# Kernel tuning notes

Measured on AMD Instinct MI355X. Metric: run time of the kernel, lower is better.

## Reference

```python
import jax, jax.numpy as jnp
import numpy as np

NPOINT, RADIUS, SIGMA, K = 1024, 0.1, 0.05, 32
KDE_K = 128  # N_points default of kernel_density_estimation_ball


def setup_inputs() -> dict:
    key = jax.random.key(0)
    ks = jax.random.split(key, 9)
    B, N, C = 4, 4096, 16

    def glorot(k, shape):
        fan_in, fan_out = shape
        return jax.random.normal(k, shape, jnp.float32) * jnp.sqrt(2.0 / (fan_in + fan_out))

    return {
        'xyz': jax.random.uniform(ks[0], (B, N, 3), jnp.float32),      # unit cube
        'feature': jax.random.normal(ks[1], (B, N, C), jnp.float32),
        'w_mlp0': glorot(ks[2], (3 + C, 128)),
        'w_mlp1': glorot(ks[3], (128, 128)),
        'w_mlp2': glorot(ks[4], (128, 256)),
        'w_wn': glorot(ks[5], (3, 32)),
        'w_nl0': glorot(ks[6], (1, 16)),
        'w_nl1': glorot(ks[7], (16, 1)),
        'w_np': glorot(ks[8], (32, 256)),
    }


def _pdist2(a, b):
    # squared pairwise distances [B, M, N]
    return (jnp.sum(a * a, -1)[:, :, None] + jnp.sum(b * b, -1)[:, None, :]
            - 2.0 * jnp.einsum('bmd,bnd->bmn', a, b))


def _fps(xyz, npoint):
    # farthest point sampling, seeded at index 0 (matches CUDA op semantics)
    B, N, _ = xyz.shape

    def step(carry, _):
        min_d, last = carry
        p = jnp.take_along_axis(xyz, last[:, None, None], axis=1)  # [B,1,3]
        d = jnp.sum((xyz - p) ** 2, -1)                            # [B,N]
        min_d = jnp.minimum(min_d, d)
        nxt = jnp.argmax(min_d, axis=1).astype(jnp.int32)
        return (min_d, nxt), nxt

    init = (jnp.full((B, N), jnp.inf, xyz.dtype), jnp.zeros((B,), jnp.int32))
    _, rest = jax.lax.scan(step, init, None, length=npoint - 1)
    return jnp.concatenate([jnp.zeros((B, 1), jnp.int32), rest.T], axis=1)  # [B,npoint]


def _ball_query(xyz, radius, k):
    # first-k-in-index-order neighbors with d2 < r^2, padded with first hit
    B, N, _ = xyz.shape
    d2 = _pdist2(xyz, xyz)
    in_ball = d2 < radius * radius                 # self always included
    j = jnp.arange(N, dtype=jnp.int32)
    keys = jnp.where(in_ball, j, j + N)            # in-ball indices sort first
    _, idx = jax.lax.top_k(-keys, k)               # k smallest keys -> positions j
    cnt = jnp.minimum(jnp.sum(in_ball, axis=-1), k)            # [B,N]
    valid = jnp.arange(k) < cnt[..., None]
    idx = jnp.where(valid, idx, idx[..., :1])
    return idx, cnt


def _kde_ball(xyz, radius, sigma, kde_k):
    idx, cnt = _ball_query(xyz, radius, kde_k)     # [B,N,kde_k], [B,N]
    b_ix = jnp.arange(xyz.shape[0])[:, None, None]
    g = xyz[b_ix, idx] - xyz[:, :, None, :]        # [B,N,kde_k,3]
    R = jnp.sqrt(jnp.float32(sigma))
    quad = jnp.sum(jnp.square(g / R), axis=-1)     # [B,N,kde_k]
    mvn = jnp.exp(-0.5 * quad - 3.0 * jnp.log(R) - 1.5 * jnp.log(2.0 * 3.1415926))
    first = mvn[..., :1]
    total = jnp.sum(mvn, axis=-1, keepdims=True)
    cntf = cnt.astype(xyz.dtype)[..., None]
    total = total - first * (jnp.float32(kde_k) - cntf)  # remove padded duplicates
    return total / cntf                             # [B,N,1]


def _knn(k, src, q):
    d2 = _pdist2(q, src)                            # [B,P,N]
    _, idx = jax.lax.top_k(-d2, k)                  # ascending distance
    return idx


def _forward(xyz, feature, w_mlp0, w_mlp1, w_mlp2, w_wn, w_nl0, w_nl1, w_np):
    B = xyz.shape[0]
    conv = lambda x, w: jax.nn.relu(jnp.einsum('bpkc,cf->bpkf', x, w))  # bias-free 1x1 conv

    fps_idx = _fps(xyz, NPOINT)
    new_xyz = jnp.take_along_axis(xyz, fps_idx[..., None], axis=1)      # [B,P,3]

    knn_idx = _knn(K, xyz, new_xyz)                                      # [B,P,K]
    b_ix = jnp.arange(B)[:, None, None]
    grouped_xyz = xyz[b_ix, knn_idx] - new_xyz[:, :, None, :]            # [B,P,K,3]
    grouped_feature = jnp.concatenate([grouped_xyz, feature[b_ix, knn_idx]], axis=-1)

    inv_density = 1.0 / _kde_ball(xyz, RADIUS, SIGMA, KDE_K)             # [B,N,1]
    grouped_density = inv_density[b_ix, knn_idx]                          # [B,P,K,1]
    density_scale = grouped_density / jnp.max(grouped_density, axis=2, keepdims=True)

    h = conv(conv(conv(grouped_feature, w_mlp0), w_mlp1), w_mlp2)        # [B,P,K,256]
    weight = conv(grouped_xyz, w_wn)                                      # [B,P,K,32]
    density_scale = conv(conv(density_scale, w_nl0), w_nl1)               # [B,P,K,1]

    pts = h * density_scale
    pts = jnp.einsum('bpkc,bpkw->bpcw', pts, weight)                      # [B,P,256,32]
    # np_conv: 1x1 kernel with stride [1, mlp[-1]] + VALID -> only c=0 slice survives
    out = jax.nn.relu(jnp.einsum('bpw,wf->bpf', pts[:, :, 0, :], w_np))   # [B,P,256]
    return new_xyz, out


def reference(xyz, feature, w_mlp0, w_mlp1, w_mlp2, w_wn, w_nl0, w_nl1, w_np):
    return _forward(xyz, feature, w_mlp0, w_mlp1, w_mlp2, w_wn, w_nl0, w_nl1, w_np)
```

## Files before the change

### kernel.cpp

```cpp
#include <hip/hip_runtime.h>
#include <math.h>

#pragma clang fp contract(off)

typedef float v2f __attribute__((ext_vector_type(2)));

__global__ __launch_bounds__(256) void prep_kernel(
    const float* __restrict__ xyz, const float* __restrict__ w0,
    const float* __restrict__ w1, const float* __restrict__ w2,
    float* __restrict__ norms, float* __restrict__ W0T,
    float* __restrict__ W1T, float* __restrict__ W2c,
    unsigned* __restrict__ flag)
{
    int t = blockIdx.x * 256 + threadIdx.x;
    if (t == 0) *flag = 0u;
    if (t < 16384) {
        float x = xyz[t*3+0], y = xyz[t*3+1], z = xyz[t*3+2];
        norms[t] = (x*x + y*y) + z*z;
        int c = t >> 7, k = t & 127;
        W1T[c*128 + k] = w1[k*128 + c];
    }
    if (t < 2432) { int c = t / 19, i = t - c*19; W0T[t] = w0[i*128 + c]; }
    if (t < 128)  { W2c[t] = w2[t*256]; }
}

template<int CTRL>
__device__ __forceinline__ double dpp_f64(double v) {
    int lo = __double2loint(v), hi = __double2hiint(v);
    int plo = __builtin_amdgcn_update_dpp(lo, lo, CTRL, 0xF, 0xF, false);
    int phi = __builtin_amdgcn_update_dpp(hi, hi, CTRL, 0xF, 0xF, false);
    return __hiloint2double(phi, plo);
}
template<int CTRL>
__device__ __forceinline__ double max_f64_dpp(double k) {
    return fmax(dpp_f64<CTRL>(k), k);
}
#define KD(md2bits_f, ipi) __hiloint2double(__float_as_int(md2bits_f), (int)(ipi))

__global__ __launch_bounds__(512) void fps_kde_kernel(
    const float* __restrict__ xyz, const float* __restrict__ norms,
    float* __restrict__ new_xyz, float* __restrict__ invden,
    unsigned* __restrict__ flag)
{
    __shared__ float4 pts[4096];
    __shared__ float  nxb[3072];
    __shared__ __attribute__((aligned(16))) double swkd[2][4];
    int tid = threadIdx.x;

    if (blockIdx.x < 4) {
        int b = blockIdx.x;
        const float* Xb = xyz + b*12288;
        for (int t = tid; t < 4096; t += 512)
            pts[t] = make_float4(Xb[t*3+0], Xb[t*3+1], Xb[t*3+2], 0.0f);
        __syncthreads();
        if (tid < 256) {
            int lane = tid & 63, wave = tid >> 6;
            v2f Xp[8], Yp[8], Zp[8], md2[8];
            unsigned ip[16];
#pragma unroll
            for (int k = 0; k < 8; ++k) {
                float4 A = pts[(2*k)*256 + tid];
                float4 B = pts[(2*k+1)*256 + tid];
                Xp[k].x = A.x;  Xp[k].y = B.x;
                Yp[k].x = A.y;  Yp[k].y = B.y;
                Zp[k].x = A.z;  Zp[k].y = B.z;
                md2[k].x = INFINITY; md2[k].y = INFINITY;
                ip[2*k]   = ~((unsigned)((2*k)*256 + tid));
                ip[2*k+1] = ~((unsigned)((2*k+1)*256 + tid));
            }
            float cx = pts[0].x, cy = pts[0].y, cz = pts[0].z;
            if (tid == 0) { nxb[0] = cx; nxb[1] = cy; nxb[2] = cz; }
            int buf = 0;
            for (int it = 1; it < 1024; ++it) {
                v2f cx2, cy2, cz2;
                cx2.x = cx; cx2.y = cx;
                cy2.x = cy; cy2.y = cy;
                cz2.x = cz; cz2.y = cz;
#pragma unroll
                for (int k = 0; k < 8; ++k) {
                    v2f dx = Xp[k] - cx2, dy = Yp[k] - cy2, dz = Zp[k] - cz2;
                    v2f dd = (dx*dx + dy*dy) + dz*dz;
                    md2[k] = __builtin_elementwise_min(md2[k], dd);
                }
                double t0 = fmax(fmax(KD(md2[0].x,ip[0]),  KD(md2[0].y,ip[1])),
                                 fmax(KD(md2[1].x,ip[2]),  KD(md2[1].y,ip[3])));
                double t1 = fmax(fmax(KD(md2[2].x,ip[4]),  KD(md2[2].y,ip[5])),
                                 fmax(KD(md2[3].x,ip[6]),  KD(md2[3].y,ip[7])));
                double t2 = fmax(fmax(KD(md2[4].x,ip[8]),  KD(md2[4].y,ip[9])),
                                 fmax(KD(md2[5].x,ip[10]), KD(md2[5].y,ip[11])));
                double t3 = fmax(fmax(KD(md2[6].x,ip[12]), KD(md2[6].y,ip[13])),
                                 fmax(KD(md2[7].x,ip[14]), KD(md2[7].y,ip[15])));
                double key = fmax(fmax(t0, t1), fmax(t2, t3));
                key = max_f64_dpp<0xB1>(key);
                key = max_f64_dpp<0x4E>(key);
                key = max_f64_dpp<0x141>(key);
                key = max_f64_dpp<0x140>(key);
                key = max_f64_dpp<0x142>(key);
                key = max_f64_dpp<0x143>(key);
                if (lane == 63) swkd[buf][wave] = key;
                __syncthreads();
                double2 wab = *((const double2*)&swkd[buf][0]);
                double2 wcd = *((const double2*)&swkd[buf][2]);
                double kk = fmax(fmax(wab.x, wab.y), fmax(wcd.x, wcd.y));
                int fp = (int)(~((unsigned)__double2loint(kk)));
                float4 c = pts[fp];
                cx = c.x; cy = c.y; cz = c.z;
                if (tid == 0) { nxb[it*3+0] = cx; nxb[it*3+1] = cy; nxb[it*3+2] = cz; }
                buf ^= 1;
            }
        } else {
            for (int it = 1; it < 1024; ++it) __syncthreads();
        }
        __syncthreads();
        float* NX = new_xyz + b*3072;
        for (int t = tid; t < 3072; t += 512) NX[t] = nxb[t];
        if (tid == 0)
            __hip_atomic_fetch_add(flag, 1u, __ATOMIC_RELAXED,
                                   __HIP_MEMORY_SCOPE_AGENT);
    } else if (blockIdx.x < 2052) {
        int idx = blockIdx.x - 4;
        int b = idx >> 9;
        int wave = tid >> 6, lane = tid & 63;
        int i_local = ((idx & 511) << 3) + wave;
        const float* Xb = xyz + b*12288;
        const float* Nb = norms + b*4096;
        for (int t = tid; t < 4096; t += 512)
            pts[t] = make_float4(Xb[t*3+0], Xb[t*3+1], Xb[t*3+2], Nb[t]);
        __syncthreads();
        float4 c = pts[i_local];
        const float Rv    = sqrtf(0.05f);
        const float inv_s = 1.0f / (Rv*Rv);
        const float K1    = -3.0f*logf(Rv) - 1.5f*logf(2.0f*3.1415926f);
        float csum = 0.0f; int cnt = 0;
        for (int j = lane; j < 4096; j += 64) {
            float4 q = pts[j];
            float dot = (c.x*q.x + c.y*q.y) + c.z*q.z;
            float t2 = 2.0f * dot;
            float d2 = (c.w + q.w) - t2;
            if (d2 < 0.01f) {
                float gx = q.x - c.x, gy = q.y - c.y, gz = q.z - c.z;
                float dd = (gx*gx + gy*gy) + gz*gz;
                csum += expf(-0.5f * (dd * inv_s) + K1);
                cnt  += 1;
            }
        }
#pragma unroll
        for (int m = 1; m < 64; m <<= 1) {
            csum += __shfl_xor(csum, m, 64);
            cnt  += __shfl_xor(cnt,  m, 64);
        }
        if (lane == 0) {
            float den = csum / (float)cnt;
            invden[b*4096 + i_local] = 1.0f / den;
        }
    } else {
        float a = 1.0f + (float)tid * 1e-7f;
        const float bm = 1.000001f, cm = 0.999999f;
        while (__hip_atomic_load(flag, __ATOMIC_RELAXED,
                                 __HIP_MEMORY_SCOPE_AGENT) < 4u) {
            for (int i = 0; i < 512; ++i) a = fmaf(a, bm, cm);
        }
        asm volatile("" :: "v"(a));
    }
}

__global__ __launch_bounds__(256) void knn_kernel(
    const float* __restrict__ xyz, const float* __restrict__ norms,
    const float* __restrict__ new_xyz, int* __restrict__ knn_idx)
{
    __shared__ unsigned sd2[4*4096];
    __shared__ int sIdx[4*32];
    int wave = threadIdx.x >> 6, lane = threadIdx.x & 63;
    int qg = blockIdx.x*4 + wave;
    int b = qg >> 10;
    const float* Q = new_xyz + qg*3;
    float qx = Q[0], qy = Q[1], qz = Q[2];
    float nq = (qx*qx + qy*qy) + qz*qz;
    const float* Xb = xyz + b*12288;
    const float* Nb = norms + b*4096;
    unsigned* d2w = sd2 + wave*4096;
    for (int j = lane; j < 4096; j += 64) {
        float x = Xb[j*3+0], y = Xb[j*3+1], z = Xb[j*3+2];
        float dot = (qx*x + qy*y) + qz*z;
        float t2 = 2.0f*dot;
        float d = (nq + Nb[j]) - t2;
        unsigned u = __float_as_uint(d);
        unsigned m = ((unsigned)((int)u >> 31)) | 0x80000000u;
        d2w[j] = u ^ m;
    }
    for (int r = 0; r < 32; ++r) {
        double a0 = -INFINITY, a1 = -INFINITY, a2 = -INFINITY, a3 = -INFINITY;
#pragma unroll
        for (int t = 0; t < 16; ++t) {
            int jb = t*256 + lane*4;
            uint4 v = *((const uint4*)(d2w + jb));
            a0 = fmax(a0, __hiloint2double((int)v.x, jb));
            a1 = fmax(a1, __hiloint2double((int)v.y, jb+1));
            a2 = fmax(a2, __hiloint2double((int)v.z, jb+2));
            a3 = fmax(a3, __hiloint2double((int)v.w, jb+3));
        }
        double key = fmax(fmax(a0, a1), fmax(a2, a3));
        key = max_f64_dpp<0xB1>(key);
        key = max_f64_dpp<0x4E>(key);
        key = max_f64_dpp<0x141>(key);
        key = max_f64_dpp<0x140>(key);
        key = max_f64_dpp<0x142>(key);
        key = max_f64_dpp<0x143>(key);
        int jwin = __builtin_amdgcn_readlane(__double2loint(key), 63);
        if (lane == 0) { sIdx[wave*32 + r] = jwin; d2w[jwin] = 0xFFFFFFFFu; }
    }
    if (lane < 32) knn_idx[qg*32 + lane] = sIdx[wave*32 + lane];
}

__global__ __launch_bounds__(256, 2) void group_mlp_kernel(
    const float* __restrict__ xyz, const float* __restrict__ feat,
    const float* __restrict__ new_xyz, const int* __restrict__ knn_idx,
    const float* __restrict__ invden,
    const float* __restrict__ W0T, const float* __restrict__ W1T,
    const float* __restrict__ W2c, const float* __restrict__ wwn,
    const float* __restrict__ wnl0, const float* __restrict__ wnl1,
    float* __restrict__ ptsw)
{
    int row = blockIdx.x*256 + threadIdx.x;
    int k  = row & 31;
    int pg = row >> 5;
    int b  = row >> 15;
    int j  = knn_idx[row];
    const float* Xb = xyz + b*12288;
    const float* Q  = new_xyz + pg*3;
    float in[19];
    in[0] = Xb[j*3+0] - Q[0];
    in[1] = Xb[j*3+1] - Q[1];
    in[2] = Xb[j*3+2] - Q[2];
    const float4* F = (const float4*)(feat + (size_t)(b*4096 + j)*16);
    float4 f0 = F[0], f1 = F[1], f2 = F[2], f3 = F[3];
    in[3]=f0.x; in[4]=f0.y; in[5]=f0.z; in[6]=f0.w;
    in[7]=f1.x; in[8]=f1.y; in[9]=f1.z; in[10]=f1.w;
    in[11]=f2.x; in[12]=f2.y; in[13]=f2.z; in[14]=f2.w;
    in[15]=f3.x; in[16]=f3.y; in[17]=f3.z; in[18]=f3.w;

    float gd = invden[b*4096 + j];
    float mx = gd;
#pragma unroll
    for (int m = 1; m < 32; m <<= 1) mx = fmaxf(mx, __shfl_xor(mx, m, 64));
    float dsc = gd / mx;
    float sacc = 0.0f;
#pragma unroll
    for (int t = 0; t < 16; ++t)
        sacc = fmaf(fmaxf(dsc * wnl0[t], 0.0f), wnl1[t], sacc);
    float ds = fmaxf(sacc, 0.0f);

    float h1[128];
#pragma unroll
    for (int c = 0; c < 128; ++c) {
        const float* w = W0T + c*19;
        float a = in[0]*w[0];
#pragma unroll
        for (int i = 1; i < 19; ++i) a = fmaf(in[i], w[i], a);
        h1[c] = fmaxf(a, 0.0f);
    }
    float acc0 = 0.0f;
    for (int c2 = 0; c2 < 128; ++c2) {
        const float* w = W1T + c2*128;
        float a0 = 0.0f, a1 = 0.0f, a2 = 0.0f, a3 = 0.0f;
#pragma unroll
        for (int kk = 0; kk < 128; kk += 4) {
            a0 = fmaf(h1[kk+0], w[kk+0], a0);
            a1 = fmaf(h1[kk+1], w[kk+1], a1);
            a2 = fmaf(h1[kk+2], w[kk+2], a2);
            a3 = fmaf(h1[kk+3], w[kk+3], a3);
        }
        float a = (a0+a1) + (a2+a3);
        acc0 = fmaf(fmaxf(a, 0.0f), W2c[c2], acc0);
    }
    float h0 = fmaxf(acc0, 0.0f);
    float s = h0 * ds;

    float gx = in[0], gy = in[1], gz = in[2];
    float* pw = ptsw + pg*32;
#pragma unroll
    for (int w = 0; w < 32; ++w) {
        float a = gx * wwn[w];
        a = fmaf(gy, wwn[32+w], a);
        a = fmaf(gz, wwn[64+w], a);
        float part = s * fmaxf(a, 0.0f);
#pragma unroll
        for (int m = 1; m < 32; m <<= 1) part += __shfl_xor(part, m, 64);
        if (k == 0) pw[w] = part;
    }
}

__global__ __launch_bounds__(256) void final_kernel(
    const float* __restrict__ ptsw, const float* __restrict__ wnp,
    float* __restrict__ out)
{
    int pg = blockIdx.x;
    int f  = threadIdx.x;
    const float* pw = ptsw + pg*32;
    float a = 0.0f;
#pragma unroll
    for (int w = 0; w < 32; ++w) a = fmaf(pw[w], wnp[w*256+f], a);
    out[pg*256 + f] = fmaxf(a, 0.0f);
}

extern "C" void kernel_launch(void* const* d_in, const int* in_sizes, int n_in,
                              void* d_out, int out_size, void* d_ws, size_t ws_size,
                              hipStream_t stream) {
    const float* xyz  = (const float*)d_in[0];
    const float* feat = (const float*)d_in[1];
    const float* w0   = (const float*)d_in[2];
    const float* w1   = (const float*)d_in[3];
    const float* w2   = (const float*)d_in[4];
    const float* wwn  = (const float*)d_in[5];
    const float* wnl0 = (const float*)d_in[6];
    const float* wnl1 = (const float*)d_in[7];
    const float* wnp  = (const float*)d_in[8];

    float* out_all  = (float*)d_out;
    float* new_xyz  = out_all;
    float* out2     = out_all + 12288;

    char* ws = (char*)d_ws;
    float* norms  = (float*)(ws + 0);
    float* invden = (float*)(ws + 65536);
    int*   knn    = (int*)  (ws + 131072);
    float* ptsw   = (float*)(ws + 655360);
    float* W0T    = (float*)(ws + 1179648);
    float* W1T    = (float*)(ws + 1189376);
    float* W2c    = (float*)(ws + 1254912);
    unsigned* flag = (unsigned*)ptsw;

    prep_kernel<<<64, 256, 0, stream>>>(xyz, w0, w1, w2, norms, W0T, W1T, W2c,
                                        flag);
    fps_kde_kernel<<<2556, 512, 0, stream>>>(xyz, norms, new_xyz, invden, flag);
    knn_kernel<<<1024, 256, 0, stream>>>(xyz, norms, new_xyz, knn);
    group_mlp_kernel<<<512, 256, 0, stream>>>(xyz, feat, new_xyz, knn, invden,
                                              W0T, W1T, W2c, wwn, wnl0, wnl1, ptsw);
    final_kernel<<<4096, 256, 0, stream>>>(ptsw, wnp, out2);
}
```

Measured before the change: 824.9 us.

## Use packed FP32 FMA and LDS-staged W1 in group MLP; drop spin-wait blocks

The group MLP layers now use v_pk_fma_f32 on float pairs. W0 is read directly in its original layout, which removes the W0T transpose in the prep kernel. The 64KB W1T matrix is copied into shared memory per block and read as float4. Separately, the extra blocks of the FPS/KDE kernel that spun on an atomic flag while FPS ran are removed, along with the flag. The packed math aims to roughly halve the FMA instruction count in the dominant MLP. The risks are lower occupancy from the 64KB of LDS per block and losing whatever clock or scheduling effect the spinning blocks had.

```diff
diff --git a/kernel.cpp b/kernel.cpp
--- a/kernel.cpp
+++ b/kernel.cpp
@@ -4,23 +4,26 @@
 #pragma clang fp contract(off)
 
 typedef float v2f __attribute__((ext_vector_type(2)));
+
+__device__ __forceinline__ v2f pk_fma(v2f a, v2f b, v2f c) {
+    v2f d;
+    asm("v_pk_fma_f32 %0, %1, %2, %3" : "=v"(d) : "v"(a), "v"(b), "v"(c));
+    return d;
+}
 
 __global__ __launch_bounds__(256) void prep_kernel(
     const float* __restrict__ xyz, const float* __restrict__ w0,
     const float* __restrict__ w1, const float* __restrict__ w2,
-    float* __restrict__ norms, float* __restrict__ W0T,
-    float* __restrict__ W1T, float* __restrict__ W2c,
-    unsigned* __restrict__ flag)
+    float* __restrict__ norms, float* __restrict__ W1T,
+    float* __restrict__ W2c)
 {
     int t = blockIdx.x * 256 + threadIdx.x;
-    if (t == 0) *flag = 0u;
     if (t < 16384) {
         float x = xyz[t*3+0], y = xyz[t*3+1], z = xyz[t*3+2];
         norms[t] = (x*x + y*y) + z*z;
         int c = t >> 7, k = t & 127;
         W1T[c*128 + k] = w1[k*128 + c];
     }
-    if (t < 2432) { int c = t / 19, i = t - c*19; W0T[t] = w0[i*128 + c]; }
     if (t < 128)  { W2c[t] = w2[t*256]; }
 }
 
@@ -39,8 +42,7 @@
 
 __global__ __launch_bounds__(512) void fps_kde_kernel(
     const float* __restrict__ xyz, const float* __restrict__ norms,
-    float* __restrict__ new_xyz, float* __restrict__ invden,
-    unsigned* __restrict__ flag)
+    float* __restrict__ new_xyz, float* __restrict__ invden)
 {
     __shared__ float4 pts[4096];
     __shared__ float  nxb[3072];
@@ -114,10 +116,7 @@
         __syncthreads();
         float* NX = new_xyz + b*3072;
         for (int t = tid; t < 3072; t += 512) NX[t] = nxb[t];
-        if (tid == 0)
-            __hip_atomic_fetch_add(flag, 1u, __ATOMIC_RELAXED,
-                                   __HIP_MEMORY_SCOPE_AGENT);
-    } else if (blockIdx.x < 2052) {
+    } else {
         int idx = blockIdx.x - 4;
         int b = idx >> 9;
         int wave = tid >> 6, lane = tid & 63;
@@ -153,14 +152,6 @@
             float den = csum / (float)cnt;
             invden[b*4096 + i_local] = 1.0f / den;
         }
-    } else {
-        float a = 1.0f + (float)tid * 1e-7f;
-        const float bm = 1.000001f, cm = 0.999999f;
-        while (__hip_atomic_load(flag, __ATOMIC_RELAXED,
-                                 __HIP_MEMORY_SCOPE_AGENT) < 4u) {
-            for (int i = 0; i < 512; ++i) a = fmaf(a, bm, cm);
-        }
-        asm volatile("" :: "v"(a));
     }
 }
 
@@ -216,11 +207,20 @@
     const float* __restrict__ xyz, const float* __restrict__ feat,
     const float* __restrict__ new_xyz, const int* __restrict__ knn_idx,
     const float* __restrict__ invden,
-    const float* __restrict__ W0T, const float* __restrict__ W1T,
+    const float* __restrict__ w0, const float* __restrict__ W1T,
     const float* __restrict__ W2c, const float* __restrict__ wwn,
     const float* __restrict__ wnl0, const float* __restrict__ wnl1,
     float* __restrict__ ptsw)
 {
+    __shared__ float sW1[16384];
+    {
+        const float4* g4 = (const float4*)W1T;
+        float4* s4 = (float4*)sW1;
+#pragma unroll
+        for (int i = 0; i < 16; ++i)
+            s4[i*256 + threadIdx.x] = g4[i*256 + threadIdx.x];
+    }
+
     int row = blockIdx.x*256 + threadIdx.x;
     int k  = row & 31;
     int pg = row >> 5;
@@ -250,27 +250,36 @@
         sacc = fmaf(fmaxf(dsc * wnl0[t], 0.0f), wnl1[t], sacc);
     float ds = fmaxf(sacc, 0.0f);
 
-    float h1[128];
-#pragma unroll
-    for (int c = 0; c < 128; ++c) {
-        const float* w = W0T + c*19;
-        float a = in[0]*w[0];
-#pragma unroll
-        for (int i = 1; i < 19; ++i) a = fmaf(in[i], w[i], a);
-        h1[c] = fmaxf(a, 0.0f);
-    }
+    v2f h1v[64];
+    const v2f* W0v = (const v2f*)w0;
+#pragma unroll
+    for (int cc = 0; cc < 64; ++cc) {
+        v2f in0; in0.x = in[0]; in0.y = in[0];
+        v2f acc = in0 * W0v[cc];
+#pragma unroll
+        for (int i = 1; i < 19; ++i) {
+            v2f ini; ini.x = in[i]; ini.y = in[i];
+            acc = pk_fma(ini, W0v[i*64 + cc], acc);
+        }
+        v2f z; z.x = 0.0f; z.y = 0.0f;
+        h1v[cc] = __builtin_elementwise_max(acc, z);
+    }
+    __syncthreads();
+
     float acc0 = 0.0f;
     for (int c2 = 0; c2 < 128; ++c2) {
-        const float* w = W1T + c2*128;
-        float a0 = 0.0f, a1 = 0.0f, a2 = 0.0f, a3 = 0.0f;
-#pragma unroll
-        for (int kk = 0; kk < 128; kk += 4) {
-            a0 = fmaf(h1[kk+0], w[kk+0], a0);
-            a1 = fmaf(h1[kk+1], w[kk+1], a1);
-            a2 = fmaf(h1[kk+2], w[kk+2], a2);
-            a3 = fmaf(h1[kk+3], w[kk+3], a3);
-        }
-        float a = (a0+a1) + (a2+a3);
+        const float4* w4 = (const float4*)(sW1 + c2*128);
+        v2f a01; a01.x = 0.0f; a01.y = 0.0f;
+        v2f a23; a23.x = 0.0f; a23.y = 0.0f;
+#pragma unroll
+        for (int kk = 0; kk < 32; ++kk) {
+            float4 wv = w4[kk];
+            v2f wab; wab.x = wv.x; wab.y = wv.y;
+            v2f wcd; wcd.x = wv.z; wcd.y = wv.w;
+            a01 = pk_fma(h1v[2*kk],   wab, a01);
+            a23 = pk_fma(h1v[2*kk+1], wcd, a23);
+        }
+        float a = (a01.x + a01.y) + (a23.x + a23.y);
         acc0 = fmaf(fmaxf(a, 0.0f), W2c[c2], acc0);
     }
     float h0 = fmaxf(acc0, 0.0f);
@@ -325,16 +334,14 @@
     float* invden = (float*)(ws + 65536);
     int*   knn    = (int*)  (ws + 131072);
     float* ptsw   = (float*)(ws + 655360);
-    float* W0T    = (float*)(ws + 1179648);
     float* W1T    = (float*)(ws + 1189376);
     float* W2c    = (float*)(ws + 1254912);
-    unsigned* flag = (unsigned*)ptsw;
-
-    prep_kernel<<<64, 256, 0, stream>>>(xyz, w0, w1, w2, norms, W0T, W1T, W2c,
-                                        flag);
-    fps_kde_kernel<<<2556, 512, 0, stream>>>(xyz, norms, new_xyz, invden, flag);
+
+    prep_kernel<<<64, 256, 0, stream>>>(xyz, w0, w1, w2, norms, W1T, W2c);
+    fps_kde_kernel<<<2052, 512, 0, stream>>>(xyz, norms, new_xyz, invden);
     knn_kernel<<<1024, 256, 0, stream>>>(xyz, norms, new_xyz, knn);
     group_mlp_kernel<<<512, 256, 0, stream>>>(xyz, feat, new_xyz, knn, invden,
-                                              W0T, W1T, W2c, wwn, wnl0, wnl1, ptsw);
+                                              w0, W1T, W2c, wwn, wnl0, wnl1,
+                                              ptsw);
     final_kernel<<<4096, 256, 0, stream>>>(ptsw, wnp, out2);
 }
```

Result: faster. 796.5 us (-3.4%).
